# Kernel tuning notes

Measured on AMD Instinct MI355X. Metric: run time of the kernel, lower is better.

Reference implementation:

```python
import jax, jax.numpy as jnp
import numpy as np

START = 1  # strings_utils.SpecialSymbol.START
B, S, H, V = 16, 256, 512, 32000

def setup_inputs() -> dict:
    key = jax.random.key(0)
    ks = jax.random.split(key, 8)
    sc = 1.0 / np.sqrt(H)
    return {
        "target": jax.random.randint(ks[0], (B, S), 0, V, dtype=jnp.int64),
        "hidden_state": jax.random.normal(ks[1], (1, B, H), jnp.float32),
        "cell_state": jax.random.normal(ks[2], (1, B, H), jnp.float32),
        "embedding": jax.random.normal(ks[3], (V, H), jnp.float32) * 0.02,  # tied with out.weight
        "W_ih": jax.random.uniform(ks[4], (4 * H, H), jnp.float32, -sc, sc),
        "W_hh": jax.random.uniform(ks[5], (4 * H, H), jnp.float32, -sc, sc),
        "b_ih": jax.random.uniform(ks[6], (4 * H,), jnp.float32, -sc, sc),
        "b_hh": jax.random.uniform(ks[7], (4 * H,), jnp.float32, -sc, sc),
        "out_bias": jnp.zeros((V,), jnp.float32),
    }

def reference(target, hidden_state, cell_state, embedding, W_ih, W_hh, b_ih, b_hh, out_bias):
    # Teacher-forced decode: input at step 0 is START, then target[:, :-1]
    tokens = jnp.concatenate(
        [jnp.full((target.shape[0], 1), START, dtype=target.dtype), target[:, :-1]], axis=1
    )  # [B, S]
    emb = embedding[tokens]  # [B, S, H]
    # Precompute input contribution to gates for all steps (one big GEMM)
    xW = jnp.einsum("bsh,gh->bsg", emb, W_ih) + b_ih + b_hh  # [B, S, 4H]
    h0, c0 = hidden_state[0], cell_state[0]  # num_layers == 1

    def step(carry, x_t):
        h, c = carry
        gates = x_t + h @ W_hh.T  # [B, 4H]
        i, f, g, o = jnp.split(gates, 4, axis=-1)  # torch gate order: i, f, g, o
        i, f, o = jax.nn.sigmoid(i), jax.nn.sigmoid(f), jax.nn.sigmoid(o)
        g = jnp.tanh(g)
        c = f * c + i * g
        h = o * jnp.tanh(c)
        return (h, c), h

    (_, _), hs = jax.lax.scan(step, (h0, c0), jnp.swapaxes(xW, 0, 1))  # hs: [S, B, H]
    hs = jnp.swapaxes(hs, 0, 1)  # [B, S, H]
    logits = jnp.einsum("bsh,vh->bsv", hs, embedding) + out_bias  # tied projection [B, S, V]
    return logits
```

## Files before the change

kernel.cpp:

```cpp
#include <hip/hip_runtime.h>
#include <stdint.h>

#define B_N 16
#define S_N 256
#define H_N 512
#define V_N 32000
#define G4_N 2048
#define START_TOK 1
#define NBLK 16
#define UPB 32
#define ROWS 128

typedef float f32x4 __attribute__((ext_vector_type(4)));
typedef int   i32x4 __attribute__((ext_vector_type(4)));
typedef unsigned short u16;
typedef u16 u16x4 __attribute__((ext_vector_type(4)));
typedef unsigned u32x2 __attribute__((ext_vector_type(2)));

static __device__ __forceinline__ u16 f2bf(float f) {
  unsigned u = __float_as_uint(f);
  return (u16)((u + 0x7fffu + ((u >> 16) & 1u)) >> 16);
}
static __device__ __forceinline__ float bf2f(u16 b) {
  return __uint_as_float(((unsigned)b) << 16);
}

static __device__ __forceinline__ void mfma_av(f32x4& d, i32x4 a, i32x4 b) {
  asm("v_mfma_f32_16x16x32_bf16 %0, %1, %2, %0" : "+v"(d) : "a"(a), "v"(b));
}
static __device__ __forceinline__ void mfma_vv(f32x4& d, i32x4 a, i32x4 b) {
  asm("v_mfma_f32_16x16x32_bf16 %0, %1, %2, %0" : "+v"(d) : "v"(a), "v"(b));
}

static __device__ __forceinline__ void async16(const void* g, void* l) {
  __builtin_amdgcn_global_load_lds((const __attribute__((address_space(1))) unsigned*)g,
                                   (__attribute__((address_space(3))) unsigned*)l,
                                   16, 0, 0);
}

static __device__ __forceinline__ f32x4 llc16(const float* p) {
  f32x4 v;
  asm volatile("global_load_dwordx4 %0, %1, off sc0 sc1" : "=v"(v) : "v"(p));
  return v;
}

static __device__ __forceinline__ float vexp2(float x) {
  float r; asm("v_exp_f32 %0, %1\n\ts_nop 1" : "=v"(r) : "v"(x)); return r;
}
static __device__ __forceinline__ float vrcp(float x) {
  float r; asm("v_rcp_f32 %0, %1\n\ts_nop 1" : "=v"(r) : "v"(x)); return r;
}
static __device__ __forceinline__ float fsig(float x) {
  return vrcp(1.f + vexp2(-1.44269504f * x));
}
static __device__ __forceinline__ float ftanh(float x) {
  return 1.f - 2.f * vrcp(1.f + vexp2(2.88539008f * x));
}


__global__ void cast_bf16_kernel(const float* __restrict__ in, u16* __restrict__ out, int n4) {
  int i = blockIdx.x * blockDim.x + threadIdx.x;
  int stride = gridDim.x * blockDim.x;
  for (int q = i; q < n4; q += stride) {
    f32x4 v = *(const f32x4*)(in + 4l * q);
    u16x4 o;
    o.x = f2bf(v.x); o.y = f2bf(v.y); o.z = f2bf(v.z); o.w = f2bf(v.w);
    *(u16x4*)(out + 4l * q) = o;
  }
}

__global__ void zero_ctr_kernel(unsigned* __restrict__ ctr) {
  ctr[threadIdx.x] = 0u;
}


template<bool GATHER>
__global__ __launch_bounds__(256)
void gemm_bf16_128(const u16* __restrict__ A, const u16* __restrict__ Bm,
                   float* __restrict__ C, int N,
                   const float* __restrict__ bias0, const float* __restrict__ bias1,
                   const int* __restrict__ target) {
  constexpr int K = H_N;
  __shared__ u16 Alds[128 * 32];
  __shared__ u16 Blds[128 * 32];
  const int tid  = threadIdx.x;
  const int lane = tid & 63;
  const int wq   = tid >> 6;
  const int mbase = blockIdx.y * 128;
  const int nbase = blockIdx.x * 128;

  const int r     = tid >> 2;
  const int off16 = (tid & 3) << 4;

  long arow0, arow1;
  if (GATHER) {
    int m0 = mbase + r, m1 = mbase + 64 + r;
    int t0 = m0 & (S_N - 1), b0 = m0 >> 8;
    int t1 = m1 & (S_N - 1), b1 = m1 >> 8;
    arow0 = (t0 == 0) ? START_TOK : target[b0 * S_N + t0 - 1];
    arow1 = (t1 == 0) ? START_TOK : target[b1 * S_N + t1 - 1];
  } else {
    arow0 = mbase + r;
    arow1 = mbase + 64 + r;
  }
  const long brow0 = nbase + r, brow1 = nbase + 64 + r;

  char* AldsB = (char*)Alds;
  char* BldsB = (char*)Blds;
  const char* Ab = (const char*)A;
  const char* Bb = (const char*)Bm;
  const int ldsw = wq << 10;

  const int wm   = (wq >> 1) << 6;
  const int wn   = (wq & 1) << 6;
  const int lrow = lane & 15;
  const int lk   = (lane >> 4) << 3;

  f32x4 acc[4][4] = {};

  for (int kt = 0; kt < K / 32; ++kt) {
    __syncthreads();
    const long kb = kt * 64 + off16;
    async16(Ab + arow0 * (K * 2) + kb, AldsB + ldsw);
    async16(Ab + arow1 * (K * 2) + kb, AldsB + 4096 + ldsw);
    async16(Bb + brow0 * (K * 2) + kb, BldsB + ldsw);
    async16(Bb + brow1 * (K * 2) + kb, BldsB + 4096 + ldsw);
    __syncthreads();

    i32x4 a[4], b[4];
    #pragma unroll
    for (int mi = 0; mi < 4; ++mi)
      a[mi] = *(const i32x4*)(AldsB + (((wm + mi * 16 + lrow) << 5) + lk) * 2);
    #pragma unroll
    for (int ni = 0; ni < 4; ++ni)
      b[ni] = *(const i32x4*)(BldsB + (((wn + ni * 16 + lrow) << 5) + lk) * 2);
    #pragma unroll
    for (int mi = 0; mi < 4; ++mi)
      #pragma unroll
      for (int ni = 0; ni < 4; ++ni)
        mfma_vv(acc[mi][ni], a[mi], b[ni]);
  }
  asm volatile("s_nop 7\n\ts_nop 7");

  const int rbase = (lane >> 4) << 2;
  #pragma unroll
  for (int ni = 0; ni < 4; ++ni) {
    const int col = nbase + wn + ni * 16 + lrow;
    float bv = bias0[col];
    if (bias1) bv += bias1[col];
    #pragma unroll
    for (int mi = 0; mi < 4; ++mi) {
      const int row = mbase + wm + mi * 16 + rbase;
      f32x4 v = acc[mi][ni];
      if (GATHER) {
        int b  = row >> 8, s0 = row & (S_N - 1);
        int g  = col >> 9, blkc = (col >> 5) & 15, uu = col & 31;
        size_t base = (((size_t)s0 * 16 + blkc) * 4 + g) * 512 + b * 32 + uu;
        C[base]         = v.x + bv;
        C[base + 32768] = v.y + bv;
        C[base + 65536] = v.z + bv;
        C[base + 98304] = v.w + bv;
      } else {
        C[(long)(row + 0) * N + col] = v.x + bv;
        C[(long)(row + 1) * N + col] = v.y + bv;
        C[(long)(row + 2) * N + col] = v.z + bv;
        C[(long)(row + 3) * N + col] = v.w + bv;
      }
    }
  }
}


__global__ __launch_bounds__(256, 1)
void lstm_scan_coop(const float* __restrict__ xWt, const u16* __restrict__ Whh16,
                    const float* __restrict__ h0, const float* __restrict__ c0,
                    unsigned* __restrict__ hbuf, unsigned* __restrict__ ctr,
                    unsigned* __restrict__ hs32) {
  __shared__ __align__(16) u16 hl_hi[B_N * H_N];
  __shared__ __align__(16) u16 hl_lo[B_N * H_N];
  __shared__ __align__(16) float glT[16 * 132];

  const int blk  = blockIdx.x;
  const int tid  = threadIdx.x;
  const int lane = tid & 63;
  const int wv   = tid >> 6;
  const int u0   = blk * UPB;
  char* hiB = (char*)hl_hi;
  char* loB = (char*)hl_lo;

  i32x4 afr[2][16];
  {
    const char* Wb = (const char*)Whh16;
    #pragma unroll
    for (int t = 0; t < 2; ++t) {
      int r = wv * 32 + t * 16 + (lane & 15);
      long grow = (long)(r >> 5) * H_N + u0 + (r & 31);
      const char* rowp = Wb + grow * (H_N * 2) + ((lane >> 4) << 4);
      #pragma unroll
      for (int kt = 0; kt < 16; ++kt)
        afr[t][kt] = *(const i32x4*)(rowp + kt * 64);
    }
  }

  const int u  = tid & 31;
  const int b0 = tid >> 5;
  float c_[2];
  c_[0] = c0[(b0)     * H_N + u0 + u];
  c_[1] = c0[(b0 + 8) * H_N + u0 + u];

  #pragma unroll
  for (int q = 0; q < 8; ++q) {
    int cidx = (q * 256 + tid) * 4;
    f32x4 v = *(const f32x4*)(h0 + cidx);
    int b = cidx >> 9, j0 = (cidx & 511) >> 1;
    u16 h0a = f2bf(v.x), h1a = f2bf(v.y), h2a = f2bf(v.z), h3a = f2bf(v.w);
    u32x2 hw, lw;
    hw.x = (unsigned)h0a | ((unsigned)h1a << 16);
    hw.y = (unsigned)h2a | ((unsigned)h3a << 16);
    lw.x = (unsigned)f2bf(v.x - bf2f(h0a)) | ((unsigned)f2bf(v.y - bf2f(h1a)) << 16);
    lw.y = (unsigned)f2bf(v.z - bf2f(h2a)) | ((unsigned)f2bf(v.w - bf2f(h3a)) << 16);
    unsigned wa = (unsigned)(b * 1024 + j0 * 4) ^ ((unsigned)(b & 7) << 4);
    *(u32x2*)(hiB + wa) = hw;
    *(u32x2*)(loB + wa) = lw;
  }
  __syncthreads();

  const unsigned hrow  = (unsigned)(lane & 15);
  const unsigned hbase = hrow * 1024;
  const unsigned hswz  = (hrow & 7) << 4;
  const unsigned ksub  = ((unsigned)(lane >> 4)) << 4;

  for (int s = 0; s < S_N; ++s) {
    const float* xb = xWt + (size_t)s * 32768 + blk * 2048 + b0 * 32 + u;
    float x00 = xb[0],   x01 = xb[512], x02 = xb[1024], x03 = xb[1536];
    float x10 = xb[256], x11 = xb[768], x12 = xb[1280], x13 = xb[1792];

    f32x4 a00 = {0.f,0.f,0.f,0.f}, a01 = {0.f,0.f,0.f,0.f};
    f32x4 a10 = {0.f,0.f,0.f,0.f}, a11 = {0.f,0.f,0.f,0.f};
    #pragma unroll
    for (int kt = 0; kt < 16; ++kt) {
      unsigned off = (hbase + (unsigned)(kt * 64) + ksub) ^ hswz;
      i32x4 bhi = *(const i32x4*)(hiB + off);
      i32x4 blo = *(const i32x4*)(loB + off);
      mfma_av(a00, afr[0][kt], bhi);
      mfma_av(a10, afr[1][kt], bhi);
      mfma_av(a01, afr[0][kt], blo);
      mfma_av(a11, afr[1][kt], blo);
    }
    asm volatile("s_nop 7\n\ts_nop 7\n\ts_nop 7");

    f32x4 g0 = a00 + a01;
    f32x4 g1 = a10 + a11;
    {
      int bc = lane & 15, ks = lane >> 4;
      float* p0 = glT + bc * 132 + wv * 32 + ks * 4;
      *(f32x4*)(p0)      = g0;
      *(f32x4*)(p0 + 16) = g1;
    }
    __syncthreads();

    #pragma unroll
    for (int p = 0; p < 2; ++p) {
      const int bb = b0 + p * 8;
      const float* gp = glT + bb * 132 + u;
      float gi = gp[0]  + (p ? x10 : x00);
      float gf = gp[32] + (p ? x11 : x01);
      float gg = gp[64] + (p ? x12 : x02);
      float go = gp[96] + (p ? x13 : x03);
      gi = fsig(gi); gf = fsig(gf); gg = ftanh(gg); go = fsig(go);
      c_[p] = gf * c_[p] + gi * gg;
      float hv = go * ftanh(c_[p]);

      unsigned hb16  = (unsigned)f2bf(hv);
      unsigned other = (unsigned)__shfl_xor((int)hb16, 1);
      if ((u & 1) == 0)
        hs32[((size_t)(bb * S_N + s) * H_N + u0 + u) >> 1] = hb16 | (other << 16);

      if (s < S_N - 1)
        __hip_atomic_store(&hbuf[(s & 1) * (B_N * H_N) + bb * H_N + u0 + u],
                           __float_as_uint(hv), __ATOMIC_RELAXED, __HIP_MEMORY_SCOPE_AGENT);
    }

    if (s == S_N - 1) break;

    __syncthreads();
    if (tid == 0) {
      __hip_atomic_fetch_add(&ctr[s], 1u, __ATOMIC_RELAXED, __HIP_MEMORY_SCOPE_AGENT);
      while (__hip_atomic_load(&ctr[s], __ATOMIC_RELAXED, __HIP_MEMORY_SCOPE_AGENT) < NBLK)
        __builtin_amdgcn_s_sleep(1);
    }
    __syncthreads();

    const float* hb = (const float*)hbuf + (s & 1) * (B_N * H_N);
    f32x4 tv[8];
    #pragma unroll
    for (int q = 0; q < 8; ++q)
      tv[q] = llc16(hb + (q * 256 + tid) * 4);
    asm volatile("s_waitcnt vmcnt(0)" ::: "memory");
    __builtin_amdgcn_sched_barrier(0);
    #pragma unroll
    for (int q = 0; q < 8; ++q) {
      int cidx = (q * 256 + tid) * 4;
      int b = cidx >> 9, j0 = (cidx & 511) >> 1;
      f32x4 v = tv[q];
      u16 h0a = f2bf(v.x), h1a = f2bf(v.y), h2a = f2bf(v.z), h3a = f2bf(v.w);
      u32x2 hw, lw;
      hw.x = (unsigned)h0a | ((unsigned)h1a << 16);
      hw.y = (unsigned)h2a | ((unsigned)h3a << 16);
      lw.x = (unsigned)f2bf(v.x - bf2f(h0a)) | ((unsigned)f2bf(v.y - bf2f(h1a)) << 16);
      lw.y = (unsigned)f2bf(v.z - bf2f(h2a)) | ((unsigned)f2bf(v.w - bf2f(h3a)) << 16);
      unsigned wa = (unsigned)(b * 1024 + j0 * 4) ^ ((unsigned)(b & 7) << 4);
      *(u32x2*)(hiB + wa) = hw;
      *(u32x2*)(loB + wa) = lw;
    }
    __syncthreads();
  }
}


extern "C" void kernel_launch(void* const* d_in, const int* in_sizes, int n_in,
                              void* d_out, int out_size, void* d_ws, size_t ws_size,
                              hipStream_t stream) {
  const int*   target = (const int*)  d_in[0];
  const float* h0     = (const float*)d_in[1];
  const float* c0     = (const float*)d_in[2];
  const float* emb    = (const float*)d_in[3];
  const float* W_ih   = (const float*)d_in[4];
  const float* W_hh   = (const float*)d_in[5];
  const float* b_ih   = (const float*)d_in[6];
  const float* b_hh   = (const float*)d_in[7];
  const float* out_b  = (const float*)d_in[8];
  float* out = (float*)d_out;

  char* ws = (char*)d_ws;
  u16*      E16   = (u16*)     (ws);
  u16*      Wih16 = (u16*)     (ws + 32768000);
  u16*      Whh16 = (u16*)     (ws + 34865152);
  float*    xWt   = (float*)   (ws + 36962304);
  u16*      hs16  = (u16*)     (ws + 70516736);
  unsigned* hbuf  = (unsigned*)(ws + 74711040);
  unsigned* ctr   = (unsigned*)(ws + 74776576);
  (void)ws_size; (void)in_sizes; (void)n_in; (void)out_size;

  cast_bf16_kernel<<<2048, 256, 0, stream>>>(emb,  E16,   (V_N * H_N) / 4);
  cast_bf16_kernel<<<1024, 256, 0, stream>>>(W_ih, Wih16, (G4_N * H_N) / 4);
  cast_bf16_kernel<<<1024, 256, 0, stream>>>(W_hh, Whh16, (G4_N * H_N) / 4);
  zero_ctr_kernel <<<1, 256, 0, stream>>>(ctr);

  gemm_bf16_128<true><<<dim3(G4_N / 128, (B_N * S_N) / 128), 256, 0, stream>>>(
      E16, Wih16, xWt, G4_N, b_ih, b_hh, target);

  lstm_scan_coop<<<NBLK, 256, 0, stream>>>(xWt, Whh16, h0, c0, hbuf, ctr,
                                           (unsigned*)hs16);

  gemm_bf16_128<false><<<dim3(V_N / 128, (B_N * S_N) / 128), 256, 0, stream>>>(
      hs16, E16, out, V_N, out_b, nullptr, nullptr);
}
```

Baseline: 1.262 ms.

## Interleave gate rows per wave to drop LDS gate exchange and pre-split h exchange

```diff
diff --git a/kernel.cpp b/kernel.cpp
--- a/kernel.cpp
+++ b/kernel.cpp
@@ -8,14 +8,11 @@
 #define G4_N 2048
 #define START_TOK 1
 #define NBLK 16
-#define UPB 32
-#define ROWS 128
 
 typedef float f32x4 __attribute__((ext_vector_type(4)));
 typedef int   i32x4 __attribute__((ext_vector_type(4)));
 typedef unsigned short u16;
 typedef u16 u16x4 __attribute__((ext_vector_type(4)));
-typedef unsigned u32x2 __attribute__((ext_vector_type(2)));
 
 static __device__ __forceinline__ u16 f2bf(float f) {
   unsigned u = __float_as_uint(f);
@@ -38,8 +35,8 @@
                                    16, 0, 0);
 }
 
-static __device__ __forceinline__ f32x4 llc16(const float* p) {
-  f32x4 v;
+static __device__ __forceinline__ i32x4 llc16(const void* p) {
+  i32x4 v;
   asm volatile("global_load_dwordx4 %0, %1, off sc0 sc1" : "=v"(v) : "v"(p));
   return v;
 }
@@ -69,8 +66,16 @@
   }
 }
 
-__global__ void zero_ctr_kernel(unsigned* __restrict__ ctr) {
-  ctr[threadIdx.x] = 0u;
+__global__ void init_scan_kernel(const float* __restrict__ h0, unsigned* __restrict__ Phi,
+                                 unsigned* __restrict__ Plo, unsigned* __restrict__ ctr) {
+  int i = blockIdx.x * blockDim.x + threadIdx.x;
+  if (i < 256) ctr[i] = 0u;
+  float f0 = h0[2 * i];
+  float f1 = h0[2 * i + 1];
+  u16 h0a = f2bf(f0), h1a = f2bf(f1);
+  u16 l0a = f2bf(f0 - bf2f(h0a)), l1a = f2bf(f1 - bf2f(h1a));
+  Phi[i] = (unsigned)h0a | ((unsigned)h1a << 16);
+  Plo[i] = (unsigned)l0a | ((unsigned)l1a << 16);
 }
 
 
@@ -154,8 +159,8 @@
       f32x4 v = acc[mi][ni];
       if (GATHER) {
         int b  = row >> 8, s0 = row & (S_N - 1);
-        int g  = col >> 9, blkc = (col >> 5) & 15, uu = col & 31;
-        size_t base = (((size_t)s0 * 16 + blkc) * 4 + g) * 512 + b * 32 + uu;
+        int ug = col & 511, g = col >> 9;
+        size_t base = (((size_t)s0 * 64 + (ug >> 3)) * 16 + b) * 32 + (ug & 7) * 4 + g;
         C[base]         = v.x + bv;
         C[base + 32768] = v.y + bv;
         C[base + 65536] = v.z + bv;
@@ -173,18 +178,20 @@
 
 __global__ __launch_bounds__(256, 1)
 void lstm_scan_coop(const float* __restrict__ xWt, const u16* __restrict__ Whh16,
-                    const float* __restrict__ h0, const float* __restrict__ c0,
-                    unsigned* __restrict__ hbuf, unsigned* __restrict__ ctr,
+                    const float* __restrict__ c0, unsigned* __restrict__ Phi,
+                    unsigned* __restrict__ Plo, unsigned* __restrict__ ctr,
                     unsigned* __restrict__ hs32) {
   __shared__ __align__(16) u16 hl_hi[B_N * H_N];
   __shared__ __align__(16) u16 hl_lo[B_N * H_N];
-  __shared__ __align__(16) float glT[16 * 132];
 
   const int blk  = blockIdx.x;
   const int tid  = threadIdx.x;
   const int lane = tid & 63;
   const int wv   = tid >> 6;
-  const int u0   = blk * UPB;
+  const int wid  = blk * 4 + wv;
+  const int fr   = lane & 15;
+  const int ksub = lane >> 4;
+  const int b    = fr;
   char* hiB = (char*)hl_hi;
   char* loB = (char*)hl_lo;
 
@@ -193,53 +200,57 @@
     const char* Wb = (const char*)Whh16;
     #pragma unroll
     for (int t = 0; t < 2; ++t) {
-      int r = wv * 32 + t * 16 + (lane & 15);
-      long grow = (long)(r >> 5) * H_N + u0 + (r & 31);
-      const char* rowp = Wb + grow * (H_N * 2) + ((lane >> 4) << 4);
+      long grow = (long)(fr & 3) * H_N + wid * 8 + t * 4 + (fr >> 2);
+      const char* rowp = Wb + grow * (H_N * 2) + ksub * 16;
       #pragma unroll
       for (int kt = 0; kt < 16; ++kt)
         afr[t][kt] = *(const i32x4*)(rowp + kt * 64);
     }
   }
 
-  const int u  = tid & 31;
-  const int b0 = tid >> 5;
-  float c_[2];
-  c_[0] = c0[(b0)     * H_N + u0 + u];
-  c_[1] = c0[(b0 + 8) * H_N + u0 + u];
-
-  #pragma unroll
-  for (int q = 0; q < 8; ++q) {
-    int cidx = (q * 256 + tid) * 4;
-    f32x4 v = *(const f32x4*)(h0 + cidx);
-    int b = cidx >> 9, j0 = (cidx & 511) >> 1;
-    u16 h0a = f2bf(v.x), h1a = f2bf(v.y), h2a = f2bf(v.z), h3a = f2bf(v.w);
-    u32x2 hw, lw;
-    hw.x = (unsigned)h0a | ((unsigned)h1a << 16);
-    hw.y = (unsigned)h2a | ((unsigned)h3a << 16);
-    lw.x = (unsigned)f2bf(v.x - bf2f(h0a)) | ((unsigned)f2bf(v.y - bf2f(h1a)) << 16);
-    lw.y = (unsigned)f2bf(v.z - bf2f(h2a)) | ((unsigned)f2bf(v.w - bf2f(h3a)) << 16);
-    unsigned wa = (unsigned)(b * 1024 + j0 * 4) ^ ((unsigned)(b & 7) << 4);
-    *(u32x2*)(hiB + wa) = hw;
-    *(u32x2*)(loB + wa) = lw;
+  const int ua = wid * 8 + ksub;
+  const int ub = ua + 4;
+  float ca = c0[b * H_N + ua];
+  float cb = c0[b * H_N + ub];
+
+  const bool stlane = ((ksub & 1) == 0);
+  const int  pua    = wid * 4 + (ksub >> 1);
+
+  {
+    i32x4 th[4], tl[4];
+    #pragma unroll
+    for (int q = 0; q < 4; ++q) {
+      int cidx = (q * 256 + tid) * 4;
+      th[q] = llc16(Phi + cidx);
+      tl[q] = llc16(Plo + cidx);
+    }
+    asm volatile("s_waitcnt vmcnt(0)" ::: "memory");
+    __builtin_amdgcn_sched_barrier(0);
+    #pragma unroll
+    for (int q = 0; q < 4; ++q) {
+      int cidx = (q * 256 + tid) * 4;
+      int bb = cidx >> 8, j = cidx & 255;
+      unsigned wa = (unsigned)(bb * 1024 + j * 4) ^ ((unsigned)(bb & 7) << 4);
+      *(i32x4*)(hiB + wa) = th[q];
+      *(i32x4*)(loB + wa) = tl[q];
+    }
   }
   __syncthreads();
 
-  const unsigned hrow  = (unsigned)(lane & 15);
-  const unsigned hbase = hrow * 1024;
-  const unsigned hswz  = (hrow & 7) << 4;
-  const unsigned ksub  = ((unsigned)(lane >> 4)) << 4;
+  const unsigned hbase = (unsigned)(fr * 1024);
+  const unsigned hswz  = ((unsigned)(fr & 7)) << 4;
+  const unsigned k16   = ((unsigned)ksub) << 4;
 
   for (int s = 0; s < S_N; ++s) {
-    const float* xb = xWt + (size_t)s * 32768 + blk * 2048 + b0 * 32 + u;
-    float x00 = xb[0],   x01 = xb[512], x02 = xb[1024], x03 = xb[1536];
-    float x10 = xb[256], x11 = xb[768], x12 = xb[1280], x13 = xb[1792];
+    const float* xp = xWt + ((size_t)s * 64 + wid) * 512 + b * 32;
+    f32x4 xwa = *(const f32x4*)(xp + ksub * 4);
+    f32x4 xwb = *(const f32x4*)(xp + 16 + ksub * 4);
 
     f32x4 a00 = {0.f,0.f,0.f,0.f}, a01 = {0.f,0.f,0.f,0.f};
     f32x4 a10 = {0.f,0.f,0.f,0.f}, a11 = {0.f,0.f,0.f,0.f};
     #pragma unroll
     for (int kt = 0; kt < 16; ++kt) {
-      unsigned off = (hbase + (unsigned)(kt * 64) + ksub) ^ hswz;
+      unsigned off = (hbase + (unsigned)(kt * 64) + k16) ^ hswz;
       i32x4 bhi = *(const i32x4*)(hiB + off);
       i32x4 blo = *(const i32x4*)(loB + off);
       mfma_av(a00, afr[0][kt], bhi);
@@ -249,36 +260,38 @@
     }
     asm volatile("s_nop 7\n\ts_nop 7\n\ts_nop 7");
 
-    f32x4 g0 = a00 + a01;
-    f32x4 g1 = a10 + a11;
-    {
-      int bc = lane & 15, ks = lane >> 4;
-      float* p0 = glT + bc * 132 + wv * 32 + ks * 4;
-      *(f32x4*)(p0)      = g0;
-      *(f32x4*)(p0 + 16) = g1;
-    }
-    __syncthreads();
-
-    #pragma unroll
-    for (int p = 0; p < 2; ++p) {
-      const int bb = b0 + p * 8;
-      const float* gp = glT + bb * 132 + u;
-      float gi = gp[0]  + (p ? x10 : x00);
-      float gf = gp[32] + (p ? x11 : x01);
-      float gg = gp[64] + (p ? x12 : x02);
-      float go = gp[96] + (p ? x13 : x03);
-      gi = fsig(gi); gf = fsig(gf); gg = ftanh(gg); go = fsig(go);
-      c_[p] = gf * c_[p] + gi * gg;
-      float hv = go * ftanh(c_[p]);
-
-      unsigned hb16  = (unsigned)f2bf(hv);
-      unsigned other = (unsigned)__shfl_xor((int)hb16, 1);
-      if ((u & 1) == 0)
-        hs32[((size_t)(bb * S_N + s) * H_N + u0 + u) >> 1] = hb16 | (other << 16);
-
-      if (s < S_N - 1)
-        __hip_atomic_store(&hbuf[(s & 1) * (B_N * H_N) + bb * H_N + u0 + u],
-                           __float_as_uint(hv), __ATOMIC_RELAXED, __HIP_MEMORY_SCOPE_AGENT);
+    f32x4 ga = a00 + a01;
+    f32x4 gb = a10 + a11;
+
+    float gia = fsig(ga.x + xwa.x), gfa = fsig(ga.y + xwa.y);
+    float gga = ftanh(ga.z + xwa.z), goa = fsig(ga.w + xwa.w);
+    ca = gfa * ca + gia * gga;
+    float ha = goa * ftanh(ca);
+
+    float gib = fsig(gb.x + xwb.x), gfb = fsig(gb.y + xwb.y);
+    float ggb = ftanh(gb.z + xwb.z), gob = fsig(gb.w + xwb.w);
+    cb = gfb * cb + gib * ggb;
+    float hb = gob * ftanh(cb);
+
+    u16 ha16 = f2bf(ha), hb16 = f2bf(hb);
+    u16 la16 = f2bf(ha - bf2f(ha16));
+    u16 lb16 = f2bf(hb - bf2f(hb16));
+
+    unsigned pha = (unsigned)ha16 | ((unsigned)__shfl_xor((int)(unsigned)ha16, 16) << 16);
+    unsigned phb = (unsigned)hb16 | ((unsigned)__shfl_xor((int)(unsigned)hb16, 16) << 16);
+    unsigned pla = (unsigned)la16 | ((unsigned)__shfl_xor((int)(unsigned)la16, 16) << 16);
+    unsigned plb = (unsigned)lb16 | ((unsigned)__shfl_xor((int)(unsigned)lb16, 16) << 16);
+
+    if (stlane) {
+      hs32[((size_t)b * S_N + s) * (H_N / 2) + pua]     = pha;
+      hs32[((size_t)b * S_N + s) * (H_N / 2) + pua + 2] = phb;
+      if (s < S_N - 1) {
+        const size_t pb = ((size_t)((s + 1) & 1) * B_N + b) * (H_N / 2);
+        __hip_atomic_store(&Phi[pb + pua],     pha, __ATOMIC_RELAXED, __HIP_MEMORY_SCOPE_AGENT);
+        __hip_atomic_store(&Phi[pb + pua + 2], phb, __ATOMIC_RELAXED, __HIP_MEMORY_SCOPE_AGENT);
+        __hip_atomic_store(&Plo[pb + pua],     pla, __ATOMIC_RELAXED, __HIP_MEMORY_SCOPE_AGENT);
+        __hip_atomic_store(&Plo[pb + pua + 2], plb, __ATOMIC_RELAXED, __HIP_MEMORY_SCOPE_AGENT);
+      }
     }
 
     if (s == S_N - 1) break;
@@ -291,27 +304,25 @@
     }
     __syncthreads();
 
-    const float* hb = (const float*)hbuf + (s & 1) * (B_N * H_N);
-    f32x4 tv[8];
-    #pragma unroll
-    for (int q = 0; q < 8; ++q)
-      tv[q] = llc16(hb + (q * 256 + tid) * 4);
-    asm volatile("s_waitcnt vmcnt(0)" ::: "memory");
-    __builtin_amdgcn_sched_barrier(0);
-    #pragma unroll
-    for (int q = 0; q < 8; ++q) {
-      int cidx = (q * 256 + tid) * 4;
-      int b = cidx >> 9, j0 = (cidx & 511) >> 1;
-      f32x4 v = tv[q];
-      u16 h0a = f2bf(v.x), h1a = f2bf(v.y), h2a = f2bf(v.z), h3a = f2bf(v.w);
-      u32x2 hw, lw;
-      hw.x = (unsigned)h0a | ((unsigned)h1a << 16);
-      hw.y = (unsigned)h2a | ((unsigned)h3a << 16);
-      lw.x = (unsigned)f2bf(v.x - bf2f(h0a)) | ((unsigned)f2bf(v.y - bf2f(h1a)) << 16);
-      lw.y = (unsigned)f2bf(v.z - bf2f(h2a)) | ((unsigned)f2bf(v.w - bf2f(h3a)) << 16);
-      unsigned wa = (unsigned)(b * 1024 + j0 * 4) ^ ((unsigned)(b & 7) << 4);
-      *(u32x2*)(hiB + wa) = hw;
-      *(u32x2*)(loB + wa) = lw;
+    {
+      const unsigned slotoff = (unsigned)(((s + 1) & 1) * 4096);
+      i32x4 th[4], tl[4];
+      #pragma unroll
+      for (int q = 0; q < 4; ++q) {
+        int cidx = (q * 256 + tid) * 4;
+        th[q] = llc16(Phi + slotoff + cidx);
+        tl[q] = llc16(Plo + slotoff + cidx);
+      }
+      asm volatile("s_waitcnt vmcnt(0)" ::: "memory");
+      __builtin_amdgcn_sched_barrier(0);
+      #pragma unroll
+      for (int q = 0; q < 4; ++q) {
+        int cidx = (q * 256 + tid) * 4;
+        int bb = cidx >> 8, j = cidx & 255;
+        unsigned wa = (unsigned)(bb * 1024 + j * 4) ^ ((unsigned)(bb & 7) << 4);
+        *(i32x4*)(hiB + wa) = th[q];
+        *(i32x4*)(loB + wa) = tl[q];
+      }
     }
     __syncthreads();
   }
@@ -338,19 +349,20 @@
   u16*      Whh16 = (u16*)     (ws + 34865152);
   float*    xWt   = (float*)   (ws + 36962304);
   u16*      hs16  = (u16*)     (ws + 70516736);
-  unsigned* hbuf  = (unsigned*)(ws + 74711040);
+  unsigned* Phi   = (unsigned*)(ws + 74711040);
+  unsigned* Plo   = (unsigned*)(ws + 74743808);
   unsigned* ctr   = (unsigned*)(ws + 74776576);
   (void)ws_size; (void)in_sizes; (void)n_in; (void)out_size;
 
   cast_bf16_kernel<<<2048, 256, 0, stream>>>(emb,  E16,   (V_N * H_N) / 4);
   cast_bf16_kernel<<<1024, 256, 0, stream>>>(W_ih, Wih16, (G4_N * H_N) / 4);
   cast_bf16_kernel<<<1024, 256, 0, stream>>>(W_hh, Whh16, (G4_N * H_N) / 4);
-  zero_ctr_kernel <<<1, 256, 0, stream>>>(ctr);
+  init_scan_kernel<<<16, 256, 0, stream>>>(h0, Phi, Plo, ctr);
 
   gemm_bf16_128<true><<<dim3(G4_N / 128, (B_N * S_N) / 128), 256, 0, stream>>>(
       E16, Wih16, xWt, G4_N, b_ih, b_hh, target);
 
-  lstm_scan_coop<<<NBLK, 256, 0, stream>>>(xWt, Whh16, h0, c0, hbuf, ctr,
+  lstm_scan_coop<<<NBLK, 256, 0, stream>>>(xWt, Whh16, c0, Phi, Plo, ctr,
                                            (unsigned*)hs16);
 
   gemm_bf16_128<false><<<dim3(V_N / 128, (B_N * S_N) / 128), 256, 0, stream>>>(
```

After: 1.214 ms. 1.04x faster.
